# Performance work log

Measured on AMD Instinct MI355X. Metric: run time of the kernel, lower is better.

Reference implementation:

```python
import jax, jax.numpy as jnp
import numpy as np

N = 100_000      # num_nodes
E = 3_200_000    # num_edges (avg degree 32)
F_IN = 8         # node_features
H = 64           # hidden_size
EPS = 1e-5       # batchnorm eps


def setup_inputs() -> dict:
    key = jax.random.key(0)
    ks = jax.random.split(key, 12)
    s = 0.05
    inp = {
        "x": jax.random.normal(ks[0], (N, F_IN), dtype=jnp.float32),
        "edge_index": jax.random.randint(ks[1], (2, E), 0, N, dtype=jnp.int32),
        "edge_weight": jax.random.uniform(ks[2], (E,), dtype=jnp.float32),
        # GCNConv 1: in -> hidden
        "W1": jax.random.normal(ks[3], (F_IN, H), dtype=jnp.float32) * s,
        "b1": jnp.zeros((H,), jnp.float32),
        # GCNConv 2: hidden -> hidden
        "W2": jax.random.normal(ks[4], (H, H), dtype=jnp.float32) * s,
        "b2": jnp.zeros((H,), jnp.float32),
        # BatchNorm1d (eval mode: running stats)
        "bn1_gamma": jnp.ones((H,), jnp.float32), "bn1_beta": jnp.zeros((H,), jnp.float32),
        "bn1_mean": jnp.zeros((H,), jnp.float32), "bn1_var": jnp.ones((H,), jnp.float32),
        "bn2_gamma": jnp.ones((H,), jnp.float32), "bn2_beta": jnp.zeros((H,), jnp.float32),
        "bn2_mean": jnp.zeros((H,), jnp.float32), "bn2_var": jnp.ones((H,), jnp.float32),
        # LSTM 1: input 2H -> hidden H (window=1, zero init state => W_hh contributes nothing)
        "Wih1": jax.random.normal(ks[5], (4 * H, 2 * H), jnp.float32) * s,
        "bih1": jnp.zeros((4 * H,), jnp.float32), "bhh1": jnp.zeros((4 * H,), jnp.float32),
        # LSTM 2: input H -> hidden H
        "Wih2": jax.random.normal(ks[6], (4 * H, H), jnp.float32) * s,
        "bih2": jnp.zeros((4 * H,), jnp.float32), "bhh2": jnp.zeros((4 * H,), jnp.float32),
        # final Linear(2H + F_IN -> 1)
        "Wlin": jax.random.normal(ks[7], (2 * H + F_IN, 1), jnp.float32) * s,
        "blin": jnp.zeros((1,), jnp.float32),
    }
    return inp


def _gcn_conv(x, src, dst, w, W, b):
    # PyG GCNConv: linear, then sym-normalized propagation with self-loops (weight 1), then bias.
    h = x @ W                                                   # [N, H]
    deg = jnp.zeros((N,), h.dtype).at[dst].add(w) + 1.0         # weighted in-degree + self-loop
    dinv = jax.lax.rsqrt(deg)
    norm = dinv[src] * w * dinv[dst]                            # [E]
    agg = jax.ops.segment_sum(norm[:, None] * h[src], dst, num_segments=N)
    agg = agg + h * (1.0 / deg)[:, None]                        # self-loop term (norm = 1/deg)
    return agg + b


def _bn_eval(x, gamma, beta, mean, var):
    return (x - mean) * jax.lax.rsqrt(var + EPS) * gamma + beta


def _lstm_step0(x, Wih, bih, bhh):
    # single LSTM step from (h0, c0) = 0; PyTorch gate order i, f, g, o
    g = x @ Wih.T + (bih + bhh)
    i, f, gg, o = jnp.split(g, 4, axis=1)
    c = jax.nn.sigmoid(i) * jnp.tanh(gg)
    return jax.nn.sigmoid(o) * jnp.tanh(c)


def reference(x, edge_index, edge_weight,
              W1, b1, W2, b2,
              bn1_gamma, bn1_beta, bn1_mean, bn1_var,
              bn2_gamma, bn2_beta, bn2_mean, bn2_var,
              Wih1, bih1, bhh1, Wih2, bih2, bhh2,
              Wlin, blin):
    src, dst = edge_index[0], edge_index[1]
    # MPNNLSTM (window=1, eval: dropout disabled, batchnorm uses running stats)
    h1 = _bn_eval(jax.nn.relu(_gcn_conv(x, src, dst, edge_weight, W1, b1)),
                  bn1_gamma, bn1_beta, bn1_mean, bn1_var)
    h2 = _bn_eval(jax.nn.relu(_gcn_conv(h1, src, dst, edge_weight, W2, b2)),
                  bn2_gamma, bn2_beta, bn2_mean, bn2_var)
    feats = jnp.concatenate([h1, h2], axis=1)                   # [N, 2H]
    lh1 = _lstm_step0(feats, Wih1, bih1, bhh1)                  # [N, H]
    lh2 = _lstm_step0(lh1, Wih2, bih2, bhh2)                    # [N, H]
    Hcat = jnp.concatenate([lh1, lh2, x], axis=1)               # [N, 2H + F_IN]  (S == x for window=1)
    return jax.nn.relu(Hcat) @ Wlin + blin                      # [N, 1]
```

## Files before the change

kernel.cpp:

```cpp
#include <hip/hip_runtime.h>

#define BN_EPS 1e-5f
#define FX_SCALE 16777216.0f
#define VAL_MASK 0xFFFFFFFFFFULL
#define CNT_SHIFT 40

typedef __bf16 bf16x8 __attribute__((ext_vector_type(8)));
typedef float f32x4 __attribute__((ext_vector_type(4)));

__device__ __forceinline__ float sigf(float x) { return 1.0f / (1.0f + __expf(-x)); }
__device__ __forceinline__ float tanh_fast(float x) {
    float t = __expf(-2.0f * fabsf(x));
    float r = (1.0f - t) / (1.0f + t);
    return copysignf(r, x);
}

__global__ void k_deg(const int* __restrict__ ei, const float* __restrict__ w,
                      unsigned long long* __restrict__ cell,
                      unsigned short* __restrict__ rank, int E) {
    int i = blockIdx.x * 256 + threadIdx.x;
    if (i < E) {
        int d = ei[E + i];
        unsigned int fx = (unsigned int)(w[i] * FX_SCALE + 0.5f);
        unsigned long long add = ((unsigned long long)1 << CNT_SHIFT) | (unsigned long long)fx;
        unsigned long long old = atomicAdd(&cell[d], add);
        rank[i] = (unsigned short)(old >> CNT_SHIFT);
    }
}

__global__ void k_node(const unsigned long long* __restrict__ cell,
                       float* __restrict__ dinv, float* __restrict__ invd, int N) {
    int i = blockIdx.x * 256 + threadIdx.x;
    if (i < N) {
        float sumw = (float)(cell[i] & VAL_MASK) * (1.0f / FX_SCALE);
        float d = sumw + 1.0f;
        dinv[i] = rsqrtf(d);
        invd[i] = 1.0f / d;
    }
}

__global__ void k_scanA(const unsigned long long* __restrict__ cell,
                        int* __restrict__ rowstart, int* __restrict__ bsum, int n) {
    __shared__ int ws[4];
    int tid = threadIdx.x;
    int i0 = blockIdx.x * 1024 + tid * 4;
    int v0 = (i0     < n) ? (int)(cell[i0]     >> CNT_SHIFT) : 0;
    int v1 = (i0 + 1 < n) ? (int)(cell[i0 + 1] >> CNT_SHIFT) : 0;
    int v2 = (i0 + 2 < n) ? (int)(cell[i0 + 2] >> CNT_SHIFT) : 0;
    int v3 = (i0 + 3 < n) ? (int)(cell[i0 + 3] >> CNT_SHIFT) : 0;
    int s = v0 + v1 + v2 + v3;
    int lane = tid & 63, wid = tid >> 6;
    int inc = s;
    #pragma unroll
    for (int off = 1; off < 64; off <<= 1) {
        int t = __shfl_up(inc, off, 64);
        if (lane >= off) inc += t;
    }
    if (lane == 63) ws[wid] = inc;
    __syncthreads();
    int wpref = 0;
    #pragma unroll
    for (int k = 0; k < 4; ++k) if (k < wid) wpref += ws[k];
    int excl = wpref + inc - s;
    if (i0     < n) rowstart[i0]     = excl;
    if (i0 + 1 < n) rowstart[i0 + 1] = excl + v0;
    if (i0 + 2 < n) rowstart[i0 + 2] = excl + v0 + v1;
    if (i0 + 3 < n) rowstart[i0 + 3] = excl + v0 + v1 + v2;
    if (tid == 255) bsum[blockIdx.x] = wpref + inc;
}

__global__ void k_scanB(int* __restrict__ bsum, int nchunk) {
    __shared__ int ws[4];
    int tid = threadIdx.x;
    int v = (tid < nchunk) ? bsum[tid] : 0;
    int lane = tid & 63, wid = tid >> 6;
    int inc = v;
    #pragma unroll
    for (int off = 1; off < 64; off <<= 1) {
        int t = __shfl_up(inc, off, 64);
        if (lane >= off) inc += t;
    }
    if (lane == 63) ws[wid] = inc;
    __syncthreads();
    int wpref = 0;
    #pragma unroll
    for (int k = 0; k < 4; ++k) if (k < wid) wpref += ws[k];
    if (tid < nchunk) bsum[tid] = wpref + inc - v;
    if (tid == 255) bsum[nchunk] = ws[0] + ws[1] + ws[2] + ws[3];
}

__global__ void k_scanC(int* __restrict__ rowstart, const int* __restrict__ bsum,
                        int n, int nchunk) {
    int i = blockIdx.x * 256 + threadIdx.x;
    if (i < n) rowstart[i] += bsum[i >> 10];
    if (i == 0) rowstart[n] = bsum[nchunk];
}

__global__ void k_fill(const int* __restrict__ ei, const float* __restrict__ w,
                       const float* __restrict__ dinv, const int* __restrict__ rowstart,
                       const unsigned short* __restrict__ rank,
                       unsigned long long* __restrict__ csr, int E) {
    int i = blockIdx.x * 256 + threadIdx.x;
    if (i < E) {
        int s = ei[i], d = ei[E + i];
        int pos = rowstart[d] + (int)rank[i];
        float coef = dinv[s] * w[i] * dinv[d];
        csr[pos] = ((unsigned long long)__float_as_uint(coef) << 32) | (unsigned int)s;
    }
}

__global__ void k_prep(const float* __restrict__ Wih1, const float* __restrict__ bih1,
                       const float* __restrict__ bhh1, const float* __restrict__ Wih2,
                       const float* __restrict__ bih2, const float* __restrict__ bhh2,
                       const float* __restrict__ W2,
                       __bf16* __restrict__ wb1, __bf16* __restrict__ wb2,
                       __bf16* __restrict__ w2t,
                       float* __restrict__ bias1, float* __restrict__ bias2) {
    int idx = blockIdx.x * 256 + threadIdx.x;
    if (idx < 192 * 128) {
        int r = idx >> 7, k = idx & 127;
        int orig = r + (r >= 64 ? 64 : 0);
        wb1[idx] = (__bf16)Wih1[orig * 128 + k];
    }
    if (idx < 192 * 64) {
        int r = idx >> 6, k = idx & 63;
        int orig = r + (r >= 64 ? 64 : 0);
        wb2[idx] = (__bf16)Wih2[orig * 64 + k];
    }
    if (idx < 64 * 64) {
        int f = idx >> 6, k = idx & 63;
        w2t[idx] = (__bf16)W2[k * 64 + f];
    }
    if (idx < 192) {
        int orig = idx + (idx >= 64 ? 64 : 0);
        bias1[idx] = bih1[orig] + bhh1[orig];
        bias2[idx] = bih2[orig] + bhh2[orig];
    }
}

__global__ void k_lin1(const float* __restrict__ x, const float* __restrict__ W1,
                       __bf16* __restrict__ out, int N) {
    __shared__ float sW[512];
    sW[threadIdx.x] = W1[threadIdx.x];
    sW[threadIdx.x + 256] = W1[threadIdx.x + 256];
    __syncthreads();
    int lane = threadIdx.x & 63;
    int n = blockIdx.x * 4 + (threadIdx.x >> 6);
    if (n >= N) return;
    const float* xr = x + n * 8;
    float acc = 0.f;
    #pragma unroll
    for (int k = 0; k < 8; ++k) acc = fmaf(xr[k], sW[k * 64 + lane], acc);
    out[(size_t)n * 64 + lane] = (__bf16)acc;
}

__global__ __launch_bounds__(256)
void k_lin2m(const __bf16* __restrict__ hb1, const __bf16* __restrict__ w2t,
             __bf16* __restrict__ h2linb, int N) {
    __shared__ __bf16 lds[64 * 72];
    int tid = threadIdx.x, lane = tid & 63, w = tid >> 6;
    int n0 = blockIdx.x * 64;
    int lr = lane & 15, lk = lane >> 4;

    f32x4 acc[4];
    #pragma unroll
    for (int mt = 0; mt < 4; ++mt) acc[mt] = (f32x4){0.f, 0.f, 0.f, 0.f};

    const __bf16* wbase = w2t + (w * 16 + lr) * 64 + lk * 8;
    #pragma unroll
    for (int ks = 0; ks < 2; ++ks) {
        int koff = ks * 32 + lk * 8;
        bf16x8 B = *(const bf16x8*)(wbase + ks * 32);
        #pragma unroll
        for (int mt = 0; mt < 4; ++mt) {
            int node = n0 + mt * 16 + lr;
            bf16x8 A = *(const bf16x8*)(hb1 + (size_t)node * 64 + koff);
            acc[mt] = __builtin_amdgcn_mfma_f32_16x16x32_bf16(A, B, acc[mt], 0, 0, 0);
        }
    }
    int h = w * 16 + lr;
    #pragma unroll
    for (int mt = 0; mt < 4; ++mt)
        #pragma unroll
        for (int r = 0; r < 4; ++r)
            lds[(mt * 16 + lk * 4 + r) * 72 + h] = (__bf16)acc[mt][r];
    __syncthreads();
    int row = tid >> 2, q = tid & 3;
    int node = n0 + row;
    if (node < N) {
        float4* dst = (float4*)(h2linb + (size_t)node * 64 + q * 16);
        const float4* s = (const float4*)(lds + row * 72 + q * 16);
        dst[0] = s[0];
        dst[1] = s[1];
    }
}

__global__ void k_agg(const __bf16* __restrict__ hlin, const float* __restrict__ invd,
                      const int* __restrict__ rowstart, const unsigned long long* __restrict__ csr,
                      const float* __restrict__ bias,
                      const float* __restrict__ gam, const float* __restrict__ bet,
                      const float* __restrict__ mu, const float* __restrict__ var,
                      __bf16* __restrict__ hb, int N) {
    int lane = threadIdx.x & 63;
    int n = blockIdx.x * 4 + (threadIdx.x >> 6);
    if (n >= N) return;
    float acc = (float)hlin[(size_t)n * 64 + lane] * invd[n];
    int e0 = rowstart[n], e1 = rowstart[n + 1];
    int j = e0;
    for (; j + 4 <= e1; j += 4) {
        unsigned long long p0 = csr[j], p1 = csr[j + 1], p2 = csr[j + 2], p3 = csr[j + 3];
        int s0 = (int)(unsigned int)p0, s1 = (int)(unsigned int)p1;
        int s2 = (int)(unsigned int)p2, s3 = (int)(unsigned int)p3;
        float c0 = __uint_as_float((unsigned int)(p0 >> 32));
        float c1 = __uint_as_float((unsigned int)(p1 >> 32));
        float c2 = __uint_as_float((unsigned int)(p2 >> 32));
        float c3 = __uint_as_float((unsigned int)(p3 >> 32));
        float v0 = (float)hlin[(size_t)s0 * 64 + lane];
        float v1 = (float)hlin[(size_t)s1 * 64 + lane];
        float v2 = (float)hlin[(size_t)s2 * 64 + lane];
        float v3 = (float)hlin[(size_t)s3 * 64 + lane];
        acc = fmaf(c0, v0, acc);
        acc = fmaf(c1, v1, acc);
        acc = fmaf(c2, v2, acc);
        acc = fmaf(c3, v3, acc);
    }
    for (; j < e1; ++j) {
        unsigned long long p = csr[j];
        acc = fmaf(__uint_as_float((unsigned int)(p >> 32)),
                   (float)hlin[(size_t)(unsigned int)p * 64 + lane], acc);
    }
    float v = fmaxf(acc + bias[lane], 0.f);
    v = (v - mu[lane]) * rsqrtf(var[lane] + BN_EPS) * gam[lane] + bet[lane];
    hb[(size_t)n * 64 + lane] = (__bf16)v;
}

__global__ __launch_bounds__(256)
void k_lstm1(const __bf16* __restrict__ h1b, const __bf16* __restrict__ h2b,
             const __bf16* __restrict__ wb, const float* __restrict__ bias,
             const float* __restrict__ Wlin,
             __bf16* __restrict__ lhb, float* __restrict__ out, int N) {
    __shared__ __bf16 lh_lds[64 * 72];
    __shared__ float pbuf[64][4];
    int tid = threadIdx.x;
    int lane = tid & 63;
    int w = tid >> 6;
    int n0 = blockIdx.x * 64;
    int lr = lane & 15;
    int lk = lane >> 4;

    f32x4 acc[3][4];
    #pragma unroll
    for (int g = 0; g < 3; ++g)
        #pragma unroll
        for (int mt = 0; mt < 4; ++mt) acc[g][mt] = (f32x4){0.f, 0.f, 0.f, 0.f};

    const __bf16* wbase = wb + (w * 16 + lr) * 128 + lk * 8;
    #pragma unroll
    for (int ks = 0; ks < 4; ++ks) {
        int koff = ks * 32 + lk * 8;
        const __bf16* fb = (koff < 64) ? (h1b + koff) : (h2b + (koff - 64));
        bf16x8 A[4];
        #pragma unroll
        for (int mt = 0; mt < 4; ++mt) {
            int node = n0 + mt * 16 + lr;
            A[mt] = *(const bf16x8*)(fb + (size_t)node * 64);
        }
        #pragma unroll
        for (int g = 0; g < 3; ++g) {
            bf16x8 B = *(const bf16x8*)(wbase + g * 64 * 128 + ks * 32);
            #pragma unroll
            for (int mt = 0; mt < 4; ++mt)
                acc[g][mt] = __builtin_amdgcn_mfma_f32_16x16x32_bf16(A[mt], B, acc[g][mt], 0, 0, 0);
        }
    }

    int h = w * 16 + lr;
    float bI = bias[h], bG = bias[64 + h], bO = bias[128 + h];
    #pragma unroll
    for (int mt = 0; mt < 4; ++mt) {
        #pragma unroll
        for (int r = 0; r < 4; ++r) {
            int nl = mt * 16 + lk * 4 + r;
            float iv = sigf(acc[0][mt][r] + bI);
            float gv = tanh_fast(acc[1][mt][r] + bG);
            float ov = sigf(acc[2][mt][r] + bO);
            float lh = ov * tanh_fast(iv * gv);
            lh_lds[nl * 72 + h] = (__bf16)lh;
        }
    }
    __syncthreads();

    int row = tid >> 2, q = tid & 3;
    const __bf16* lrow = lh_lds + row * 72 + q * 16;
    float p = 0.f;
    #pragma unroll
    for (int c = 0; c < 16; ++c) p = fmaf(fmaxf((float)lrow[c], 0.f), Wlin[q * 16 + c], p);
    pbuf[row][q] = p;
    int node = n0 + row;
    if (node < N) {
        float4* dst = (float4*)(lhb + (size_t)node * 64 + q * 16);
        const float4* s = (const float4*)lrow;
        dst[0] = s[0];
        dst[1] = s[1];
    }
    __syncthreads();
    if (tid < 64) {
        int nd = n0 + tid;
        if (nd < N)
            out[nd] = pbuf[tid][0] + pbuf[tid][1] + pbuf[tid][2] + pbuf[tid][3];
    }
}

__global__ __launch_bounds__(256)
void k_lstm2(const __bf16* __restrict__ lhb, const float* __restrict__ xg,
             const __bf16* __restrict__ wb, const float* __restrict__ bias,
             const float* __restrict__ Wlin, const float* __restrict__ blin,
             float* __restrict__ out, int N) {
    __shared__ __bf16 lh_lds[64 * 72];
    __shared__ float pbuf[64][4];
    int tid = threadIdx.x;
    int lane = tid & 63;
    int w = tid >> 6;
    int n0 = blockIdx.x * 64;
    int lr = lane & 15;
    int lk = lane >> 4;

    f32x4 acc[3][4];
    #pragma unroll
    for (int g = 0; g < 3; ++g)
        #pragma unroll
        for (int mt = 0; mt < 4; ++mt) acc[g][mt] = (f32x4){0.f, 0.f, 0.f, 0.f};

    const __bf16* wbase = wb + (w * 16 + lr) * 64 + lk * 8;
    #pragma unroll
    for (int ks = 0; ks < 2; ++ks) {
        int koff = ks * 32 + lk * 8;
        bf16x8 A[4];
        #pragma unroll
        for (int mt = 0; mt < 4; ++mt) {
            int node = n0 + mt * 16 + lr;
            A[mt] = *(const bf16x8*)(lhb + (size_t)node * 64 + koff);
        }
        #pragma unroll
        for (int g = 0; g < 3; ++g) {
            bf16x8 B = *(const bf16x8*)(wbase + g * 64 * 64 + ks * 32);
            #pragma unroll
            for (int mt = 0; mt < 4; ++mt)
                acc[g][mt] = __builtin_amdgcn_mfma_f32_16x16x32_bf16(A[mt], B, acc[g][mt], 0, 0, 0);
        }
    }

    int h = w * 16 + lr;
    float bI = bias[h], bG = bias[64 + h], bO = bias[128 + h];
    #pragma unroll
    for (int mt = 0; mt < 4; ++mt) {
        #pragma unroll
        for (int r = 0; r < 4; ++r) {
            int nl = mt * 16 + lk * 4 + r;
            float iv = sigf(acc[0][mt][r] + bI);
            float gv = tanh_fast(acc[1][mt][r] + bG);
            float ov = sigf(acc[2][mt][r] + bO);
            float lh = ov * tanh_fast(iv * gv);
            lh_lds[nl * 72 + h] = (__bf16)lh;
        }
    }
    __syncthreads();

    int row = tid >> 2, q = tid & 3;
    const __bf16* lrow = lh_lds + row * 72 + q * 16;
    float p = 0.f;
    #pragma unroll
    for (int c = 0; c < 16; ++c) p = fmaf(fmaxf((float)lrow[c], 0.f), Wlin[64 + q * 16 + c], p);
    pbuf[row][q] = p;
    __syncthreads();
    if (tid < 64) {
        int nd = n0 + tid;
        if (nd < N) {
            float o = out[nd] + blin[0] + pbuf[tid][0] + pbuf[tid][1] + pbuf[tid][2] + pbuf[tid][3];
            const float* xr = xg + (size_t)nd * 8;
            #pragma unroll
            for (int k = 0; k < 8; ++k) o = fmaf(fmaxf(xr[k], 0.f), Wlin[128 + k], o);
            out[nd] = o;
        }
    }
}

extern "C" void kernel_launch(void* const* d_in, const int* in_sizes, int n_in,
                              void* d_out, int out_size, void* d_ws, size_t ws_size,
                              hipStream_t stream) {
    const float* x    = (const float*)d_in[0];
    const int*   ei   = (const int*)d_in[1];
    const float* ew   = (const float*)d_in[2];
    const float* W1   = (const float*)d_in[3];
    const float* b1   = (const float*)d_in[4];
    const float* W2   = (const float*)d_in[5];
    const float* b2   = (const float*)d_in[6];
    const float* bn1g = (const float*)d_in[7];
    const float* bn1b = (const float*)d_in[8];
    const float* bn1m = (const float*)d_in[9];
    const float* bn1v = (const float*)d_in[10];
    const float* bn2g = (const float*)d_in[11];
    const float* bn2b = (const float*)d_in[12];
    const float* bn2m = (const float*)d_in[13];
    const float* bn2v = (const float*)d_in[14];
    const float* Wih1 = (const float*)d_in[15];
    const float* bih1 = (const float*)d_in[16];
    const float* bhh1 = (const float*)d_in[17];
    const float* Wih2 = (const float*)d_in[18];
    const float* bih2 = (const float*)d_in[19];
    const float* bhh2 = (const float*)d_in[20];
    const float* Wlin = (const float*)d_in[21];
    const float* blin = (const float*)d_in[22];
    float* out = (float*)d_out;

    int N = in_sizes[0] / 8;
    int E = in_sizes[2];

    char* ws = (char*)d_ws;
    size_t off = 0;
    auto alloc = [&](size_t bytes) -> void* {
        void* p = ws + off;
        off = (off + bytes + 255) & ~(size_t)255;
        return p;
    };
    int nchunk = (N + 1023) / 1024;
    unsigned long long* cell = (unsigned long long*)alloc((size_t)N * 8);
    unsigned short* rank     = (unsigned short*)alloc((size_t)E * 2);
    float* dinv     = (float*)alloc((size_t)N * 4);
    float* invd     = (float*)alloc((size_t)N * 4);
    int*   rowstart = (int*)alloc((size_t)(N + 1) * 4);
    int*   bsum     = (int*)alloc((size_t)(nchunk + 1) * 4);
    unsigned long long* csr  = (unsigned long long*)alloc((size_t)E * 8);
    __bf16* h1linb  = (__bf16*)alloc((size_t)N * 64 * 2);
    __bf16* hb1     = (__bf16*)alloc((size_t)N * 64 * 2);
    __bf16* h2linb  = (__bf16*)alloc((size_t)N * 64 * 2);
    __bf16* hb2     = (__bf16*)alloc((size_t)N * 64 * 2);
    __bf16* lhb     = (__bf16*)alloc((size_t)N * 64 * 2);
    __bf16* wb1     = (__bf16*)alloc((size_t)192 * 128 * 2);
    __bf16* wb2     = (__bf16*)alloc((size_t)192 * 64 * 2);
    __bf16* w2t     = (__bf16*)alloc((size_t)64 * 64 * 2);
    float* bias1    = (float*)alloc(192 * 4);
    float* bias2    = (float*)alloc(192 * 4);

    hipMemsetAsync(cell, 0, (size_t)N * 8, stream);

    const int tb = 256;
    int gE = (E + tb - 1) / tb;
    int gN = (N + tb - 1) / tb;
    int nb4 = (N + 3) / 4;
    int nT = (N + 63) / 64;

    k_prep<<<96, tb, 0, stream>>>(Wih1, bih1, bhh1, Wih2, bih2, bhh2, W2,
                                  wb1, wb2, w2t, bias1, bias2);
    k_deg<<<gE, tb, 0, stream>>>(ei, ew, cell, rank, E);
    k_node<<<gN, tb, 0, stream>>>(cell, dinv, invd, N);
    k_scanA<<<nchunk, tb, 0, stream>>>(cell, rowstart, bsum, N);
    k_scanB<<<1, tb, 0, stream>>>(bsum, nchunk);
    k_scanC<<<gN, tb, 0, stream>>>(rowstart, bsum, N, nchunk);
    k_fill<<<gE, tb, 0, stream>>>(ei, ew, dinv, rowstart, rank, csr, E);

    k_lin1<<<nb4, tb, 0, stream>>>(x, W1, h1linb, N);
    k_agg<<<nb4, tb, 0, stream>>>(h1linb, invd, rowstart, csr,
                                  b1, bn1g, bn1b, bn1m, bn1v, hb1, N);
    k_lin2m<<<nT, tb, 0, stream>>>(hb1, w2t, h2linb, N);
    k_agg<<<nb4, tb, 0, stream>>>(h2linb, invd, rowstart, csr,
                                  b2, bn2g, bn2b, bn2m, bn2v, hb2, N);

    k_lstm1<<<nT, tb, 0, stream>>>(hb1, hb2, wb1, bias1, Wlin, lhb, out, N);
    k_lstm2<<<nT, tb, 0, stream>>>(lhb, x, wb2, bias2, Wlin, blin, out, N);
}
```

Baseline: 512.3 us.

## Build CSR via shared-memory chunked histograms instead of global 64-bit atomics

```diff
diff --git a/kernel.cpp b/kernel.cpp
--- a/kernel.cpp
+++ b/kernel.cpp
@@ -1,9 +1,9 @@
 #include <hip/hip_runtime.h>
 
 #define BN_EPS 1e-5f
-#define FX_SCALE 16777216.0f
-#define VAL_MASK 0xFFFFFFFFFFULL
-#define CNT_SHIFT 40
+#define CHUNK_SHIFT 16
+#define CHUNK (1 << CHUNK_SHIFT)
+#define RANGE 24576
 
 typedef __bf16 bf16x8 __attribute__((ext_vector_type(8)));
 typedef float f32x4 __attribute__((ext_vector_type(4)));
@@ -15,39 +15,54 @@
     return copysignf(r, x);
 }
 
-__global__ void k_deg(const int* __restrict__ ei, const float* __restrict__ w,
-                      unsigned long long* __restrict__ cell,
-                      unsigned short* __restrict__ rank, int E) {
-    int i = blockIdx.x * 256 + threadIdx.x;
-    if (i < E) {
-        int d = ei[E + i];
-        unsigned int fx = (unsigned int)(w[i] * FX_SCALE + 0.5f);
-        unsigned long long add = ((unsigned long long)1 << CNT_SHIFT) | (unsigned long long)fx;
-        unsigned long long old = atomicAdd(&cell[d], add);
-        rank[i] = (unsigned short)(old >> CNT_SHIFT);
-    }
-}
-
-__global__ void k_node(const unsigned long long* __restrict__ cell,
-                       float* __restrict__ dinv, float* __restrict__ invd, int N) {
-    int i = blockIdx.x * 256 + threadIdx.x;
-    if (i < N) {
-        float sumw = (float)(cell[i] & VAL_MASK) * (1.0f / FX_SCALE);
-        float d = sumw + 1.0f;
-        dinv[i] = rsqrtf(d);
-        invd[i] = 1.0f / d;
-    }
-}
-
-__global__ void k_scanA(const unsigned long long* __restrict__ cell,
+__global__ __launch_bounds__(256)
+void k_hist(const int* __restrict__ ei, unsigned* __restrict__ histg,
+            unsigned short* __restrict__ rloc, int E, int NP, int B) {
+    __shared__ unsigned hist[RANGE / 2];
+    int c = blockIdx.x % B;
+    int r = blockIdx.x / B;
+    int base = r * RANGE;
+    for (int k = threadIdx.x; k < RANGE / 2; k += 256) hist[k] = 0;
+    __syncthreads();
+    int i0 = c << CHUNK_SHIFT;
+    int iend = min(i0 + CHUNK, E);
+    for (int i = i0 + (int)threadIdx.x; i < iend; i += 256) {
+        int d = ei[E + i] - base;
+        if ((unsigned)d < (unsigned)RANGE) {
+            unsigned sh = (d & 1) * 16;
+            unsigned old = atomicAdd(&hist[d >> 1], 1u << sh);
+            rloc[i] = (unsigned short)((old >> sh) & 0xFFFFu);
+        }
+    }
+    __syncthreads();
+    unsigned* dstp = histg + ((size_t)c * NP + base) / 2;
+    for (int k = threadIdx.x; k < RANGE / 2; k += 256) dstp[k] = hist[k];
+}
+
+__global__ void k_colscan(const unsigned short* __restrict__ histg,
+                          unsigned short* __restrict__ pref, int* __restrict__ cnt,
+                          int N, int NP, int B) {
+    int d = blockIdx.x * 256 + threadIdx.x;
+    if (d >= N) return;
+    int acc = 0;
+    for (int b = 0; b < B; ++b) {
+        size_t idx = (size_t)b * NP + d;
+        int v = histg[idx];
+        pref[idx] = (unsigned short)acc;
+        acc += v;
+    }
+    cnt[d] = acc;
+}
+
+__global__ void k_scanA(const int* __restrict__ cnt,
                         int* __restrict__ rowstart, int* __restrict__ bsum, int n) {
     __shared__ int ws[4];
     int tid = threadIdx.x;
     int i0 = blockIdx.x * 1024 + tid * 4;
-    int v0 = (i0     < n) ? (int)(cell[i0]     >> CNT_SHIFT) : 0;
-    int v1 = (i0 + 1 < n) ? (int)(cell[i0 + 1] >> CNT_SHIFT) : 0;
-    int v2 = (i0 + 2 < n) ? (int)(cell[i0 + 2] >> CNT_SHIFT) : 0;
-    int v3 = (i0 + 3 < n) ? (int)(cell[i0 + 3] >> CNT_SHIFT) : 0;
+    int v0 = (i0     < n) ? cnt[i0]     : 0;
+    int v1 = (i0 + 1 < n) ? cnt[i0 + 1] : 0;
+    int v2 = (i0 + 2 < n) ? cnt[i0 + 2] : 0;
+    int v3 = (i0 + 3 < n) ? cnt[i0 + 3] : 0;
     int s = v0 + v1 + v2 + v3;
     int lane = tid & 63, wid = tid >> 6;
     int inc = s;
@@ -97,15 +112,52 @@
 }
 
 __global__ void k_fill(const int* __restrict__ ei, const float* __restrict__ w,
-                       const float* __restrict__ dinv, const int* __restrict__ rowstart,
-                       const unsigned short* __restrict__ rank,
-                       unsigned long long* __restrict__ csr, int E) {
+                       const int* __restrict__ rowstart,
+                       const unsigned short* __restrict__ rloc,
+                       const unsigned short* __restrict__ pref,
+                       unsigned long long* __restrict__ csr, int E, int NP) {
     int i = blockIdx.x * 256 + threadIdx.x;
     if (i < E) {
         int s = ei[i], d = ei[E + i];
-        int pos = rowstart[d] + (int)rank[i];
-        float coef = dinv[s] * w[i] * dinv[d];
-        csr[pos] = ((unsigned long long)__float_as_uint(coef) << 32) | (unsigned int)s;
+        int c = i >> CHUNK_SHIFT;
+        int pos = rowstart[d] + (int)pref[(size_t)c * NP + d] + (int)rloc[i];
+        csr[pos] = ((unsigned long long)__float_as_uint(w[i]) << 32) | (unsigned int)s;
+    }
+}
+
+__global__ void k_rowsum(const unsigned long long* __restrict__ csr,
+                         const int* __restrict__ rowstart,
+                         float* __restrict__ dinv, float* __restrict__ invd, int N) {
+    int lane = threadIdx.x & 63;
+    int n = blockIdx.x * 4 + (threadIdx.x >> 6);
+    if (n >= N) return;
+    int e0 = rowstart[n], e1 = rowstart[n + 1];
+    float s = 0.f;
+    for (int j = e0 + lane; j < e1; j += 64)
+        s += __uint_as_float((unsigned int)(csr[j] >> 32));
+    #pragma unroll
+    for (int off = 32; off; off >>= 1) s += __shfl_xor(s, off, 64);
+    if (lane == 0) {
+        float d = s + 1.0f;
+        dinv[n] = rsqrtf(d);
+        invd[n] = 1.0f / d;
+    }
+}
+
+__global__ void k_coef(unsigned long long* __restrict__ csr,
+                       const int* __restrict__ rowstart,
+                       const float* __restrict__ dinv, int N) {
+    int lane = threadIdx.x & 63;
+    int n = blockIdx.x * 4 + (threadIdx.x >> 6);
+    if (n >= N) return;
+    float dd = dinv[n];
+    int e0 = rowstart[n], e1 = rowstart[n + 1];
+    for (int j = e0 + lane; j < e1; j += 64) {
+        unsigned long long p = csr[j];
+        unsigned int s = (unsigned int)p;
+        float wv = __uint_as_float((unsigned int)(p >> 32));
+        float coef = dinv[s] * wv * dd;
+        csr[j] = ((unsigned long long)__float_as_uint(coef) << 32) | s;
     }
 }
 
@@ -416,6 +468,11 @@
     int N = in_sizes[0] / 8;
     int E = in_sizes[2];
 
+    int B  = (E + CHUNK - 1) >> CHUNK_SHIFT;
+    int NR = (N + RANGE - 1) / RANGE;
+    int NP = NR * RANGE;
+    int nchunk = (N + 1023) / 1024;
+
     char* ws = (char*)d_ws;
     size_t off = 0;
     auto alloc = [&](size_t bytes) -> void* {
@@ -423,9 +480,10 @@
         off = (off + bytes + 255) & ~(size_t)255;
         return p;
     };
-    int nchunk = (N + 1023) / 1024;
-    unsigned long long* cell = (unsigned long long*)alloc((size_t)N * 8);
-    unsigned short* rank     = (unsigned short*)alloc((size_t)E * 2);
+    unsigned* histg          = (unsigned*)alloc((size_t)B * NP * 2);
+    unsigned short* pref     = (unsigned short*)alloc((size_t)B * NP * 2);
+    unsigned short* rloc     = (unsigned short*)alloc((size_t)E * 2);
+    int*   cnt      = (int*)alloc((size_t)N * 4);
     float* dinv     = (float*)alloc((size_t)N * 4);
     float* invd     = (float*)alloc((size_t)N * 4);
     int*   rowstart = (int*)alloc((size_t)(N + 1) * 4);
@@ -442,8 +500,6 @@
     float* bias1    = (float*)alloc(192 * 4);
     float* bias2    = (float*)alloc(192 * 4);
 
-    hipMemsetAsync(cell, 0, (size_t)N * 8, stream);
-
     const int tb = 256;
     int gE = (E + tb - 1) / tb;
     int gN = (N + tb - 1) / tb;
@@ -452,12 +508,14 @@
 
     k_prep<<<96, tb, 0, stream>>>(Wih1, bih1, bhh1, Wih2, bih2, bhh2, W2,
                                   wb1, wb2, w2t, bias1, bias2);
-    k_deg<<<gE, tb, 0, stream>>>(ei, ew, cell, rank, E);
-    k_node<<<gN, tb, 0, stream>>>(cell, dinv, invd, N);
-    k_scanA<<<nchunk, tb, 0, stream>>>(cell, rowstart, bsum, N);
+    k_hist<<<B * NR, tb, 0, stream>>>(ei, histg, rloc, E, NP, B);
+    k_colscan<<<gN, tb, 0, stream>>>((const unsigned short*)histg, pref, cnt, N, NP, B);
+    k_scanA<<<nchunk, tb, 0, stream>>>(cnt, rowstart, bsum, N);
     k_scanB<<<1, tb, 0, stream>>>(bsum, nchunk);
     k_scanC<<<gN, tb, 0, stream>>>(rowstart, bsum, N, nchunk);
-    k_fill<<<gE, tb, 0, stream>>>(ei, ew, dinv, rowstart, rank, csr, E);
+    k_fill<<<gE, tb, 0, stream>>>(ei, ew, rowstart, rloc, pref, csr, E, NP);
+    k_rowsum<<<nb4, tb, 0, stream>>>(csr, rowstart, dinv, invd, N);
+    k_coef<<<nb4, tb, 0, stream>>>(csr, rowstart, dinv, N);
 
     k_lin1<<<nb4, tb, 0, stream>>>(x, W1, h1linb, N);
     k_agg<<<nb4, tb, 0, stream>>>(h1linb, invd, rowstart, csr,
```

New measurement: 502.3 us. About the same (-2.0%).
